# Performance work log

Hardware: AMD Instinct MI355X
Metric: run time of the kernel (lower is better)

## Reference

```python
import jax, jax.numpy as jnp
import numpy as np

EMBED_DIM = 1024
HEADS = 16
DIM_HEAD = 64  # embed_dim // heads
SCALE = DIM_HEAD ** -0.5


def setup_inputs() -> dict:
    key = jax.random.key(0)
    ks = jax.random.split(key, 6)
    x = jax.random.normal(ks[0], (2, 2048, EMBED_DIM), dtype=jnp.float32)
    # qkv_proj: Linear(embed_dim, 3*embed_dim) with bias
    w_qkv = jax.random.normal(ks[1], (EMBED_DIM, 3 * EMBED_DIM), dtype=jnp.float32) * (EMBED_DIM ** -0.5)
    b_qkv = jax.random.normal(ks[2], (3 * EMBED_DIM,), dtype=jnp.float32) * 0.01
    # out_proj: Linear(embed_dim, embed_dim) with bias
    w_out = jax.random.normal(ks[3], (EMBED_DIM, EMBED_DIM), dtype=jnp.float32) * (EMBED_DIM ** -0.5)
    b_out = jax.random.normal(ks[4], (EMBED_DIM,), dtype=jnp.float32) * 0.01
    return {"x": x, "w_qkv": w_qkv, "b_qkv": b_qkv, "w_out": w_out, "b_out": b_out}


def reference(x, w_qkv, b_qkv, w_out, b_out):
    b, s, d = x.shape
    h, dh = HEADS, d // HEADS
    qkv = x @ w_qkv + b_qkv                       # [b, s, 3d]
    qkv = qkv.reshape(b, s, 3, h, dh)
    qkv = jnp.transpose(qkv, (0, 3, 2, 1, 4))     # [b, h, 3, s, dh]
    q, k, v = qkv[:, :, 0], qkv[:, :, 1], qkv[:, :, 2]
    q = q * SCALE
    attn = jnp.einsum("bhqd,bhkd->bhqk", q, k)    # [b, h, s, s]
    attn = jax.nn.softmax(attn.astype(jnp.float32), axis=-1).astype(attn.dtype)
    # attn_dropout p=0 -> identity
    out = jnp.einsum("bhqk,bhkd->bhqd", attn, v)  # [b, h, s, dh]
    out = jnp.transpose(out, (0, 2, 1, 3)).reshape(b, s, d)
    return out @ w_out + b_out
```

## Files before the change

### kernel.cpp

```cpp
#include <hip/hip_runtime.h>

#define EMBED  1024
#define HEADS  16
#define DHEAD  64
#define SEQ    2048
#define BATCH  2
#define NTOK   4096
#define QS2    (0.125f * 1.44269504089f)
#define DEFER_THR 8.0f

typedef unsigned short u16t;
typedef float f32x4 __attribute__((ext_vector_type(4)));
typedef __bf16 bf16x8 __attribute__((ext_vector_type(8)));
typedef u16t u16x8 __attribute__((ext_vector_type(8)));
typedef u16t u16x4 __attribute__((ext_vector_type(4)));
typedef unsigned u32x4 __attribute__((ext_vector_type(4)));

static __device__ __forceinline__ u16t f2bf(float f) {
    unsigned u = __builtin_bit_cast(unsigned, f);
    return (u16t)((u + 0x7fffu + ((u >> 16) & 1u)) >> 16);
}
static __device__ __forceinline__ bf16x8 asbf(u16x8 v) {
    return __builtin_bit_cast(bf16x8, v);
}
static __device__ __forceinline__ f32x4 mfma16(bf16x8 a, bf16x8 b, f32x4 c) {
    return __builtin_amdgcn_mfma_f32_16x16x32_bf16(a, b, c, 0, 0, 0);
}
static __device__ __forceinline__ unsigned cvtpk(float lo, float hi) {
    unsigned r;
    asm("v_cvt_pk_bf16_f32 %0, %1, %2" : "=v"(r) : "v"(lo), "v"(hi));
    return r;
}

typedef const __attribute__((address_space(1))) void* as1cv;
typedef __attribute__((address_space(3))) void* as3v;
static __device__ __forceinline__ void ldsload16(const void* g, void* l) {
    __builtin_amdgcn_global_load_lds((as1cv)g, (as3v)l, 16, 0, 0);
}

__global__ __launch_bounds__(256)
void xcvt(const float* __restrict__ X, u16t* __restrict__ XB)
{
    const size_t i = ((size_t)blockIdx.x * 256 + threadIdx.x) * 8;
    float4 a = *(const float4*)&X[i];
    float4 b = *(const float4*)&X[i + 4];
    u16x8 o;
    o[0] = f2bf(a.x); o[1] = f2bf(a.y); o[2] = f2bf(a.z); o[3] = f2bf(a.w);
    o[4] = f2bf(b.x); o[5] = f2bf(b.y); o[6] = f2bf(b.z); o[7] = f2bf(b.w);
    *(u16x8*)&XB[i] = o;
}

__global__ __launch_bounds__(256)
void wtrans(const float* __restrict__ W, u16t* __restrict__ WT, int K, int N)
{
    __shared__ float L[64][65];
    const int t = threadIdx.x;
    const int k0 = blockIdx.y * 64, n0 = blockIdx.x * 64;
#pragma unroll
    for (int rep = 0; rep < 4; ++rep) {
        const int id = rep * 256 + t;
        const int kk = id >> 4, nc = (id & 15) * 4;
        float4 v = *(const float4*)&W[(size_t)(k0 + kk) * N + n0 + nc];
        L[kk][nc] = v.x; L[kk][nc + 1] = v.y; L[kk][nc + 2] = v.z; L[kk][nc + 3] = v.w;
    }
    __syncthreads();
#pragma unroll
    for (int rep = 0; rep < 2; ++rep) {
        const int id = rep * 256 + t;
        const int n = id >> 3, kc = (id & 7) * 8;
        u16x8 o;
#pragma unroll
        for (int i = 0; i < 8; ++i) o[i] = f2bf(L[kc + i][n]);
        *(u16x8*)&WT[(size_t)(n0 + n) * K + k0 + kc] = o;
    }
}

__global__ __launch_bounds__(256)
void vtrans(const u16t* __restrict__ V, u16t* __restrict__ Vt)
{
    __shared__ u16t L[64][65];
    const int t = threadIdx.x;
    const int bh = blockIdx.y;
    const int s0 = blockIdx.x * 64;
    const u16t* src = V + ((size_t)bh * SEQ + s0) * DHEAD;
#pragma unroll
    for (int rep = 0; rep < 2; ++rep) {
        const int id = rep * 256 + t;
        const int s = id >> 3, dc = (id & 7) * 8;
        u16x8 v = *(const u16x8*)&src[(size_t)s * DHEAD + dc];
#pragma unroll
        for (int i = 0; i < 8; ++i) L[s][dc + i] = v[i];
    }
    __syncthreads();
    u16t* dstb = Vt + (size_t)bh * DHEAD * SEQ + s0;
#pragma unroll
    for (int rep = 0; rep < 2; ++rep) {
        const int id = rep * 256 + t;
        const int d = id >> 3, sc = (id & 7) * 8;
        u16x8 o;
#pragma unroll
        for (int i = 0; i < 8; ++i) o[i] = L[sc + i][d];
        *(u16x8*)&dstb[(size_t)d * SEQ + sc] = o;
    }
}

__global__ __launch_bounds__(256)
void gemm_bf16(const u16t* __restrict__ A, const u16t* __restrict__ BT,
               const float* __restrict__ bias, int N, int mode,
               float* __restrict__ C0, u16t* __restrict__ Qo,
               u16t* __restrict__ Ko, u16t* __restrict__ Vo)
{
    __shared__ __align__(16) u16t Al[2][128 * 64];
    __shared__ __align__(16) u16t Bl[2][128 * 64];
    const int t = threadIdx.x;
    const int lane = t & 63;
    const int g = lane >> 4, l15 = lane & 15;
    const int w = t >> 6, wr = w >> 1, wc = w & 1;
    const int m0 = blockIdx.y * 128, n0 = blockIdx.x * 128;

    const int srow = w * 32;
    const int lrow = lane >> 3;
    const int lcol = (lane & 7) * 8;

#define GSTAGE(buf, k0)                                                          \
    {                                                                            \
        _Pragma("unroll")                                                        \
        for (int r_ = 0; r_ < 4; ++r_) {                                         \
            const int row_ = srow + r_ * 8;                                      \
            ldsload16(&A [(size_t)(m0 + row_ + lrow) * EMBED + (k0) + lcol],     \
                      &Al[buf][row_ * 64]);                                      \
            ldsload16(&BT[(size_t)(n0 + row_ + lrow) * EMBED + (k0) + lcol],     \
                      &Bl[buf][row_ * 64]);                                      \
        }                                                                        \
    }

    f32x4 acc[4][4] = {};

    GSTAGE(0, 0);
    __syncthreads();

    int cur = 0;
    for (int k0 = 0; k0 < EMBED; k0 += 64) {
        if (k0 + 64 < EMBED) GSTAGE(cur ^ 1, k0 + 64);
        const u16t* Ab = &Al[cur][0];
        const u16t* Bb = &Bl[cur][0];
#pragma unroll
        for (int kk = 0; kk < 2; ++kk) {
            bf16x8 av[4], bv[4];
#pragma unroll
            for (int i = 0; i < 4; ++i) {
                av[i] = asbf(*(const u16x8*)&Ab[(wr * 64 + i * 16 + l15) * 64 + kk * 32 + g * 8]);
                bv[i] = asbf(*(const u16x8*)&Bb[(wc * 64 + i * 16 + l15) * 64 + kk * 32 + g * 8]);
            }
#pragma unroll
            for (int i = 0; i < 4; ++i)
#pragma unroll
                for (int j = 0; j < 4; ++j)
                    acc[i][j] = mfma16(av[i], bv[j], acc[i][j]);
        }
        __syncthreads();
        cur ^= 1;
    }
#undef GSTAGE

#pragma unroll
    for (int i = 0; i < 4; ++i)
#pragma unroll
        for (int j = 0; j < 4; ++j)
#pragma unroll
            for (int r = 0; r < 4; ++r) {
                const int row = m0 + wr * 64 + i * 16 + g * 4 + r;
                const int col = n0 + wc * 64 + j * 16 + l15;
                float v = acc[i][j][r] + bias[col];
                if (mode == 0) {
                    C0[(size_t)row * N + col] = v;
                } else {
                    const int tt = col >> 10, c1 = col & 1023;
                    const int h = c1 >> 6, d = c1 & 63;
                    const int b = row >> 11, s = row & 2047;
                    if (tt == 0) v *= QS2;
                    u16t* dst = (tt == 0) ? Qo : (tt == 1 ? Ko : Vo);
                    dst[(((size_t)b * HEADS + h) * SEQ + s) * DHEAD + d] = f2bf(v);
                }
            }
}

__global__ __launch_bounds__(256)
void attn_mfma(const u16t* __restrict__ Q, const u16t* __restrict__ K,
               const u16t* __restrict__ Vt, u16t* __restrict__ AO)
{
    __shared__ __align__(16) u16t Kl[64][72];
    __shared__ __align__(16) u16t Vl[64][72];
    const int t = threadIdx.x;
    const int lane = t & 63, wq = t >> 6;
    const int g = lane >> 4, l15 = lane & 15;
    const int bh = blockIdx.y;
    const int q0 = blockIdx.x * 128;
    const int b = bh >> 4, h = bh & 15;

    const u16t* qbase = Q + ((size_t)bh * SEQ + q0 + wq * 32) * DHEAD;
    bf16x8 qf[2][2];
#pragma unroll
    for (int qh = 0; qh < 2; ++qh)
#pragma unroll
        for (int kk = 0; kk < 2; ++kk)
            qf[qh][kk] = asbf(*(const u16x8*)&qbase[(size_t)(qh * 16 + l15) * DHEAD + kk * 32 + g * 8]);

    const int srow = t >> 3, scol = (t & 7) * 8;
    const u16t* Kb = K + (size_t)bh * SEQ * DHEAD;
    const u16t* Vb = Vt + (size_t)bh * DHEAD * SEQ;

    {
        u16x8 k0r[2], v0r[2];
#pragma unroll
        for (int rep = 0; rep < 2; ++rep) {
            const int r = rep * 32 + srow;
            k0r[rep] = *(const u16x8*)&Kb[(size_t)r * DHEAD + scol];
            v0r[rep] = *(const u16x8*)&Vb[(size_t)r * SEQ + scol];
        }
#pragma unroll
        for (int rep = 0; rep < 2; ++rep) {
            const int r = rep * 32 + srow;
            *(u16x8*)&Kl[r][scol] = k0r[rep];
            *(u16x8*)&Vl[r][scol] = v0r[rep];
        }
    }
    __syncthreads();

    f32x4 accO[4][2] = {};
    float mrun[2] = {-1e30f, -1e30f}, lrun[2] = {0.f, 0.f};

    for (int kv0 = 0; kv0 < SEQ; kv0 += 64) {
        const bool more = (kv0 + 64 < SEQ);
        u16x8 kreg[2], vreg[2];
        if (more) {
#pragma unroll
            for (int rep = 0; rep < 2; ++rep) {
                const int r = rep * 32 + srow;
                kreg[rep] = *(const u16x8*)&Kb[(size_t)(kv0 + 64 + r) * DHEAD + scol];
                vreg[rep] = *(const u16x8*)&Vb[(size_t)r * SEQ + kv0 + 64 + scol];
            }
        }

        f32x4 s4[4][2] = {};
#pragma unroll
        for (int kk = 0; kk < 2; ++kk)
#pragma unroll
            for (int mf = 0; mf < 4; ++mf) {
                bf16x8 a = asbf(*(const u16x8*)&Kl[mf * 16 + l15][kk * 32 + g * 8]);
                s4[mf][0] = mfma16(a, qf[0][kk], s4[mf][0]);
                s4[mf][1] = mfma16(a, qf[1][kk], s4[mf][1]);
            }

        float mt[2];
#pragma unroll
        for (int qh = 0; qh < 2; ++qh) {
            float m = s4[0][qh][0];
#pragma unroll
            for (int mf = 0; mf < 4; ++mf)
#pragma unroll
                for (int r = 0; r < 4; ++r) m = fmaxf(m, s4[mf][qh][r]);
            m = fmaxf(m, __shfl_xor(m, 16));
            m = fmaxf(m, __shfl_xor(m, 32));
            mt[qh] = m;
        }
        const bool skip =
            __all((mt[0] - mrun[0] <= DEFER_THR) && (mt[1] - mrun[1] <= DEFER_THR)) != 0;
        float mnew[2];
#pragma unroll
        for (int qh = 0; qh < 2; ++qh)
            mnew[qh] = skip ? mrun[qh] : fmaxf(mrun[qh], mt[qh]);

        float p[4][2][4], rs[2] = {0.f, 0.f};
#pragma unroll
        for (int mf = 0; mf < 4; ++mf)
#pragma unroll
            for (int qh = 0; qh < 2; ++qh)
#pragma unroll
                for (int r = 0; r < 4; ++r) {
                    p[mf][qh][r] = __builtin_amdgcn_exp2f(s4[mf][qh][r] - mnew[qh]);
                    rs[qh] += p[mf][qh][r];
                }
#pragma unroll
        for (int qh = 0; qh < 2; ++qh) {
            rs[qh] += __shfl_xor(rs[qh], 16);
            rs[qh] += __shfl_xor(rs[qh], 32);
        }

        if (skip) {
            lrun[0] += rs[0];
            lrun[1] += rs[1];
        } else {
#pragma unroll
            for (int qh = 0; qh < 2; ++qh) {
                const float alpha = __builtin_amdgcn_exp2f(mrun[qh] - mnew[qh]);
                lrun[qh] = lrun[qh] * alpha + rs[qh];
                mrun[qh] = mnew[qh];
                float al[4];
#pragma unroll
                for (int r = 0; r < 4; ++r) al[r] = __shfl(alpha, g * 4 + r);
#pragma unroll
                for (int nf = 0; nf < 4; ++nf)
#pragma unroll
                    for (int r = 0; r < 4; ++r) accO[nf][qh][r] *= al[r];
            }
        }

        u16x8 pu[2][2];
#pragma unroll
        for (int kk = 0; kk < 2; ++kk)
#pragma unroll
            for (int qh = 0; qh < 2; ++qh) {
                const int a = kk * 2;
                u32x4 pw;
                pw[0] = cvtpk(p[a][qh][0], p[a][qh][1]);
                pw[1] = cvtpk(p[a][qh][2], p[a][qh][3]);
                pw[2] = cvtpk(p[a + 1][qh][0], p[a + 1][qh][1]);
                pw[3] = cvtpk(p[a + 1][qh][2], p[a + 1][qh][3]);
                pu[kk][qh] = __builtin_bit_cast(u16x8, pw);
            }

#pragma unroll
        for (int kk = 0; kk < 2; ++kk)
#pragma unroll
            for (int nf = 0; nf < 4; ++nf) {
                const u16t* vr = &Vl[nf * 16 + l15][0];
                u16x4 lo = *(const u16x4*)&vr[kk * 32 + g * 4];
                u16x4 hi = *(const u16x4*)&vr[kk * 32 + 16 + g * 4];
                u16x8 bb = __builtin_shufflevector(lo, hi, 0, 1, 2, 3, 4, 5, 6, 7);
                accO[nf][0] = mfma16(asbf(pu[kk][0]), asbf(bb), accO[nf][0]);
                accO[nf][1] = mfma16(asbf(pu[kk][1]), asbf(bb), accO[nf][1]);
            }

        __syncthreads();
        if (more) {
#pragma unroll
            for (int rep = 0; rep < 2; ++rep) {
                const int r = rep * 32 + srow;
                *(u16x8*)&Kl[r][scol] = kreg[rep];
                *(u16x8*)&Vl[r][scol] = vreg[rep];
            }
            __syncthreads();
        }
    }

#pragma unroll
    for (int qh = 0; qh < 2; ++qh) {
        const float inv = 1.f / lrun[qh];
        float iv[4];
#pragma unroll
        for (int r = 0; r < 4; ++r) iv[r] = __shfl(inv, g * 4 + r);
#pragma unroll
        for (int nf = 0; nf < 4; ++nf)
#pragma unroll
            for (int r = 0; r < 4; ++r) {
                const int s = q0 + wq * 32 + qh * 16 + g * 4 + r;
                AO[((size_t)b * SEQ + s) * EMBED + h * DHEAD + nf * 16 + l15] =
                    f2bf(accO[nf][qh][r] * iv[r]);
            }
    }
}

extern "C" void kernel_launch(void* const* d_in, const int* in_sizes, int n_in,
                              void* d_out, int out_size, void* d_ws, size_t ws_size,
                              hipStream_t stream)
{
    const float* x     = (const float*)d_in[0];
    const float* w_qkv = (const float*)d_in[1];
    const float* b_qkv = (const float*)d_in[2];
    const float* w_out = (const float*)d_in[3];
    const float* b_out = (const float*)d_in[4];

    u16t* xb  = (u16t*)d_ws;
    u16t* wqt = xb  + (size_t)NTOK * EMBED;
    u16t* wot = wqt + (size_t)3072 * 1024;
    u16t* Qb  = wot + (size_t)1024 * 1024;
    u16t* Kb  = Qb  + (size_t)NTOK * EMBED;
    u16t* Vb  = Kb  + (size_t)NTOK * EMBED;
    u16t* Vtb = Vb  + (size_t)NTOK * EMBED;
    u16t* AOb = Vtb + (size_t)NTOK * EMBED;

    xcvt<<<2048, 256, 0, stream>>>(x, xb);
    wtrans<<<dim3(48, 16), 256, 0, stream>>>(w_qkv, wqt, 1024, 3072);
    wtrans<<<dim3(16, 16), 256, 0, stream>>>(w_out, wot, 1024, 1024);

    gemm_bf16<<<dim3(24, 32), 256, 0, stream>>>(xb, wqt, b_qkv, 3072, 1,
                                                nullptr, Qb, Kb, Vb);
    vtrans<<<dim3(32, 32), 256, 0, stream>>>(Vb, Vtb);
    attn_mfma<<<dim3(16, 32), 256, 0, stream>>>(Qb, Kb, Vtb, AOb);
    gemm_bf16<<<dim3(8, 32), 256, 0, stream>>>(AOb, wot, b_out, 1024, 0,
                                               (float*)d_out, nullptr, nullptr, nullptr);
}
```

Baseline: 241.7 us.

## Swizzle GEMM LDS layout, drop double buffering, templatize epilogue mode

```diff
diff --git a/kernel.cpp b/kernel.cpp
--- a/kernel.cpp
+++ b/kernel.cpp
@@ -104,14 +104,15 @@
     }
 }
 
+template <int MODE>
 __global__ __launch_bounds__(256)
 void gemm_bf16(const u16t* __restrict__ A, const u16t* __restrict__ BT,
-               const float* __restrict__ bias, int N, int mode,
+               const float* __restrict__ bias, int N,
                float* __restrict__ C0, u16t* __restrict__ Qo,
                u16t* __restrict__ Ko, u16t* __restrict__ Vo)
 {
-    __shared__ __align__(16) u16t Al[2][128 * 64];
-    __shared__ __align__(16) u16t Bl[2][128 * 64];
+    __shared__ __align__(16) u16t Al[128 * 64];
+    __shared__ __align__(16) u16t Bl[128 * 64];
     const int t = threadIdx.x;
     const int lane = t & 63;
     const int g = lane >> 4, l15 = lane & 15;
@@ -120,37 +121,29 @@
 
     const int srow = w * 32;
     const int lrow = lane >> 3;
-    const int lcol = (lane & 7) * 8;
-
-#define GSTAGE(buf, k0)                                                          \
-    {                                                                            \
-        _Pragma("unroll")                                                        \
-        for (int r_ = 0; r_ < 4; ++r_) {                                         \
-            const int row_ = srow + r_ * 8;                                      \
-            ldsload16(&A [(size_t)(m0 + row_ + lrow) * EMBED + (k0) + lcol],     \
-                      &Al[buf][row_ * 64]);                                      \
-            ldsload16(&BT[(size_t)(n0 + row_ + lrow) * EMBED + (k0) + lcol],     \
-                      &Bl[buf][row_ * 64]);                                      \
-        }                                                                        \
-    }
+    const int lcolsw = ((lane & 7) ^ lrow) * 8;
+
+    const int r7 = l15 & 7;
 
     f32x4 acc[4][4] = {};
 
-    GSTAGE(0, 0);
-    __syncthreads();
-
-    int cur = 0;
     for (int k0 = 0; k0 < EMBED; k0 += 64) {
-        if (k0 + 64 < EMBED) GSTAGE(cur ^ 1, k0 + 64);
-        const u16t* Ab = &Al[cur][0];
-        const u16t* Bb = &Bl[cur][0];
+        __syncthreads();
+#pragma unroll
+        for (int r_ = 0; r_ < 4; ++r_) {
+            const int row_ = srow + r_ * 8;
+            ldsload16(&A [(size_t)(m0 + row_ + lrow) * EMBED + k0 + lcolsw], &Al[row_ * 64]);
+            ldsload16(&BT[(size_t)(n0 + row_ + lrow) * EMBED + k0 + lcolsw], &Bl[row_ * 64]);
+        }
+        __syncthreads();
 #pragma unroll
         for (int kk = 0; kk < 2; ++kk) {
             bf16x8 av[4], bv[4];
 #pragma unroll
             for (int i = 0; i < 4; ++i) {
-                av[i] = asbf(*(const u16x8*)&Ab[(wr * 64 + i * 16 + l15) * 64 + kk * 32 + g * 8]);
-                bv[i] = asbf(*(const u16x8*)&Bb[(wc * 64 + i * 16 + l15) * 64 + kk * 32 + g * 8]);
+                const int chA = ((kk * 4 + g) ^ r7) * 8;
+                av[i] = asbf(*(const u16x8*)&Al[(wr * 64 + i * 16 + l15) * 64 + chA]);
+                bv[i] = asbf(*(const u16x8*)&Bl[(wc * 64 + i * 16 + l15) * 64 + chA]);
             }
 #pragma unroll
             for (int i = 0; i < 4; ++i)
@@ -158,10 +151,7 @@
                 for (int j = 0; j < 4; ++j)
                     acc[i][j] = mfma16(av[i], bv[j], acc[i][j]);
         }
-        __syncthreads();
-        cur ^= 1;
-    }
-#undef GSTAGE
+    }
 
 #pragma unroll
     for (int i = 0; i < 4; ++i)
@@ -172,7 +162,7 @@
                 const int row = m0 + wr * 64 + i * 16 + g * 4 + r;
                 const int col = n0 + wc * 64 + j * 16 + l15;
                 float v = acc[i][j][r] + bias[col];
-                if (mode == 0) {
+                if (MODE == 0) {
                     C0[(size_t)row * N + col] = v;
                 } else {
                     const int tt = col >> 10, c1 = col & 1023;
@@ -384,10 +374,10 @@
     wtrans<<<dim3(48, 16), 256, 0, stream>>>(w_qkv, wqt, 1024, 3072);
     wtrans<<<dim3(16, 16), 256, 0, stream>>>(w_out, wot, 1024, 1024);
 
-    gemm_bf16<<<dim3(24, 32), 256, 0, stream>>>(xb, wqt, b_qkv, 3072, 1,
-                                                nullptr, Qb, Kb, Vb);
+    gemm_bf16<1><<<dim3(24, 32), 256, 0, stream>>>(xb, wqt, b_qkv, 3072,
+                                                   nullptr, Qb, Kb, Vb);
     vtrans<<<dim3(32, 32), 256, 0, stream>>>(Vb, Vtb);
     attn_mfma<<<dim3(16, 32), 256, 0, stream>>>(Qb, Kb, Vtb, AOb);
-    gemm_bf16<<<dim3(8, 32), 256, 0, stream>>>(AOb, wot, b_out, 1024, 0,
-                                               (float*)d_out, nullptr, nullptr, nullptr);
-}
+    gemm_bf16<0><<<dim3(8, 32), 256, 0, stream>>>(AOb, wot, b_out, 1024,
+                                                  (float*)d_out, nullptr, nullptr, nullptr);
+}
```

Measured after the change: 225.3 us. -6.8%, faster.
